# Optimization experiments

Hardware: AMD Instinct MI355X
Metric: run time of the kernel (lower is better)

Reference implementation:

```python
import jax, jax.numpy as jnp
import numpy as np

RADIUS = 2
TOP_K = 5000
SCORES_TH = 0.2
TEMPERATURE = 0.1


def setup_inputs() -> dict:
    key = jax.random.key(0)
    score_map = jax.random.uniform(key, (16, 1, 1024, 1024), dtype=jnp.float32)
    return {"score_map": score_map}


def _simple_nms(s, kernel_size):
    # max_pool2d(kernel, stride=1, pad=kernel//2) then keep only local maxima
    pad = kernel_size // 2
    mp = jax.lax.reduce_window(
        s, -jnp.inf, jax.lax.max,
        window_dimensions=(1, 1, kernel_size, kernel_size),
        window_strides=(1, 1, 1, 1),
        padding=((0, 0), (0, 0), (pad, pad), (pad, pad)))
    return jnp.where(s == mp, s, jnp.zeros_like(s))


def reference(score_map):
    B, _, H, W = score_map.shape
    ksize = 2 * RADIUS + 1

    # --- NMS (applied twice, as in the torch code) ---
    nms = score_map
    for _ in range(2):
        nms = _simple_nms(nms, ksize)

    # --- top-k + threshold ---
    flat = nms.reshape(B, -1)                      # (B, H*W)
    k = min(TOP_K, flat.shape[1])
    topk_scores, topk_idx = jax.lax.top_k(flat, k)  # sorted desc -> valid set is a prefix
    valid = topk_scores > SCORES_TH                 # (B, K)
    y_pix = topk_idx // W                           # (B, K) int
    x_pix = topk_idx % W

    # --- batched windowed soft-argmax refinement (boundary-aware) ---
    half = RADIUS
    d = jnp.arange(-half, half + 1)                 # (ksize,)
    dy = d[:, None] * jnp.ones((1, ksize), d.dtype) # (ksize, ksize)
    dx = d[None, :] * jnp.ones((ksize, 1), d.dtype)
    yy = y_pix[:, :, None, None] + dy               # (B, K, ksize, ksize)
    xx = x_pix[:, :, None, None] + dx
    inb = (yy >= 0) & (yy < H) & (xx >= 0) & (xx < W)
    yy_c = jnp.clip(yy, 0, H - 1)
    xx_c = jnp.clip(xx, 0, W - 1)

    sm = score_map[:, 0]                            # (B, H, W)
    b_idx = jnp.arange(B)[:, None, None, None]
    patch = sm[b_idx, yy_c, xx_c]                   # (B, K, ksize, ksize)

    # softmax over valid window entries only (out-of-bounds masked to -1e9,
    # equivalent to the torch code slicing away boundary pixels)
    logits = jnp.where(inb, patch / TEMPERATURE, jnp.float32(-1e9))
    wts = jax.nn.softmax(logits.reshape(B, k, -1), axis=-1)  # (B, K, ksize*ksize)

    dxf = dx.reshape(-1).astype(score_map.dtype)
    dyf = dy.reshape(-1).astype(score_map.dtype)
    off_x = jnp.einsum('bkw,w->bk', wts, dxf)
    off_y = jnp.einsum('bkw,w->bk', wts, dyf)

    kpts = jnp.stack([x_pix.astype(score_map.dtype) + off_x,
                      y_pix.astype(score_map.dtype) + off_y], axis=-1)  # (B, K, 2)

    # invalid (below-threshold) keypoints are zero-padded, matching the torch padding
    keypoints = jnp.where(valid[..., None], kpts, jnp.zeros_like(kpts))
    scores = jnp.where(valid, topk_scores, jnp.zeros_like(topk_scores))
    return keypoints, scores
```

## Files before the change

kernel.cpp:

```cpp
#include <hip/hip_runtime.h>
#include <math.h>

#define B 16
#define H 1024
#define W 1024
#define TOPK 5000
#define SCORES_TH 0.2f

#define SELCAP 8192
#define NB2 9831
#define OFFB2 510361
#define GS2 9840
#define SCHUNK 10

#define XSTRIPS 5
#define YSTRIPS 64
#define SROWS 16
#define SCOLS 252
#define WCAP 256
#define SLOTS (XSTRIPS * YSTRIPS)
#define CAPB (SLOTS * WCAP)

__global__ __launch_bounds__(256) void nms_wave(
    const float* __restrict__ s,
    unsigned* __restrict__ wc,
    unsigned long long* __restrict__ cand)
{
    __shared__ unsigned long long wbuf[4][WCAP];
    __shared__ unsigned wcnt[4];

    const int tid  = threadIdx.x;
    const int w    = tid >> 6;
    const int lane = tid & 63;
    const int gw   = blockIdx.x * 4 + w;
    const int xs   = gw % XSTRIPS;
    const int t    = gw / XSTRIPS;
    const int ys   = t & (YSTRIPS - 1);
    const int b    = t >> 6;
    const int slot = xs * YSTRIPS + ys;

    if (lane == 0) wcnt[w] = 0;

    const float* sb = s + (size_t)b * (H * W);
    const int c0 = xs * SCOLS - 2 + 4 * lane;
    const int y0 = ys * SROWS;
    const bool wfast = (xs > 0) & (xs < XSTRIPS - 1);

    bool inb[4], emitok[4];
    #pragma unroll
    for (int j = 0; j < 4; ++j) {
        int col = c0 + j, idx4 = 4 * lane + j;
        inb[j]    = (col >= 0) & (col < W);
        emitok[j] = inb[j] & (idx4 >= 2) & (idx4 <= 253);
    }

    float ring[4][4], p1[4], p2[4];
    #pragma unroll
    for (int j = 0; j < 4; ++j) {
        ring[j][0] = ring[j][1] = ring[j][2] = ring[j][3] = -INFINITY;
        p1[j] = p2[j] = -INFINITY;
    }

    #pragma unroll 4
    for (int gy = y0 - 2; gy <= y0 + SROWS + 1; ++gy) {
        float a[4];
        const bool yin = (gy >= 0) & (gy < H);
        if (yin & wfast) {
            float4 v = *(const float4*)(sb + (size_t)gy * W + c0);
            a[0] = v.x; a[1] = v.y; a[2] = v.z; a[3] = v.w;
        } else if (yin) {
            #pragma unroll
            for (int j = 0; j < 4; ++j)
                a[j] = inb[j] ? sb[(size_t)gy * W + c0 + j] : -INFINITY;
        } else {
            #pragma unroll
            for (int j = 0; j < 4; ++j) a[j] = -INFINITY;
        }

        float pm01 = fmaxf(a[0], a[1]);
        float pm12 = fmaxf(a[1], a[2]);
        float pm23 = fmaxf(a[2], a[3]);
        float Lh  = __shfl_up(pm23, 1);
        float La3 = __shfl_up(a[3], 1);
        float Ra0 = __shfl_down(a[0], 1);
        float Rp  = __shfl_down(pm01, 1);
        float h[4];
        h[0] = fmaxf(fmaxf(Lh,  pm01), a[2]);
        h[1] = fmaxf(fmaxf(La3, pm01), pm23);
        h[2] = fmaxf(fmaxf(pm01, pm23), Ra0);
        h[3] = fmaxf(fmaxf(pm12, pm23), Rp);

        if (gy >= y0 + 2) {
            const int r = gy - 2;
            #pragma unroll
            for (int j = 0; j < 4; ++j) {
                float vm = fmaxf(fmaxf(fmaxf(ring[j][0], ring[j][1]),
                                       fmaxf(ring[j][2], ring[j][3])), h[j]);
                bool pk = emitok[j] & (p2[j] > SCORES_TH) & (p2[j] == vm);
                if (pk) {
                    unsigned idx = (unsigned)(r * W + c0 + j);
                    unsigned long long key =
                        ((unsigned long long)__float_as_uint(p2[j]) << 32) | (unsigned)(~idx);
                    unsigned pi = atomicAdd(&wcnt[w], 1u);
                    if (pi < WCAP) wbuf[w][pi] = key;
                }
            }
        }

        #pragma unroll
        for (int j = 0; j < 4; ++j) {
            ring[j][0] = ring[j][1]; ring[j][1] = ring[j][2];
            ring[j][2] = ring[j][3]; ring[j][3] = h[j];
            p2[j] = p1[j]; p1[j] = a[j];
        }
    }

    unsigned n = wcnt[w]; if (n > WCAP) n = WCAP;
    const size_t base = (size_t)b * CAPB + (size_t)slot * WCAP;
    for (unsigned k = (unsigned)lane; k < n; k += 64)
        cand[base + k] = wbuf[w][k];
    if (lane == 0) wc[b * SLOTS + slot] = n;
}

__global__ __launch_bounds__(1024) void scan_scatter(
    const unsigned* __restrict__ wc,
    const unsigned long long* __restrict__ cand,
    unsigned* __restrict__ G,
    unsigned* __restrict__ selC,
    unsigned long long* __restrict__ sel)
{
    const int b = blockIdx.x;
    __shared__ unsigned I[NB2 + 1];
    __shared__ unsigned lwc[SLOTS];
    __shared__ unsigned wsum[16];
    __shared__ int Tsh;
    const int tid  = threadIdx.x;
    const int wv   = tid >> 6;
    const int lane = tid & 63;

    for (int i = tid; i < NB2 + 1; i += 1024) I[i] = 0;
    if (tid < SLOTS) {
        unsigned n = wc[b * SLOTS + tid];
        lwc[tid] = n > WCAP ? WCAP : n;
    }
    if (tid == 0) Tsh = 0;
    __syncthreads();

    const unsigned long long* cb = cand + (size_t)b * CAPB;

    for (unsigned i = (unsigned)tid; i < CAPB; i += 1024) {
        if ((i & (WCAP - 1)) < lwc[i >> 8]) {
            unsigned bits = (unsigned)(cb[i] >> 32);
            int bk = (int)(bits >> 11) - OFFB2;
            bk = bk < 0 ? 0 : (bk > NB2 - 1 ? NB2 - 1 : bk);
            atomicAdd(&I[bk], 1u);
        }
    }
    __syncthreads();

    unsigned local = 0;
    #pragma unroll
    for (int u = 0; u < SCHUNK; ++u) {
        int r = tid * SCHUNK + u;
        if (r < NB2) local += I[NB2 - 1 - r];
    }
    unsigned incl = local;
    #pragma unroll
    for (int off = 1; off < 64; off <<= 1) {
        unsigned v = __shfl_up(incl, off);
        if (lane >= off) incl += v;
    }
    if (lane == 63) wsum[wv] = incl;
    __syncthreads();
    if (tid < 16) {
        unsigned o = wsum[tid];
        unsigned x = o;
        #pragma unroll
        for (int off = 1; off < 16; off <<= 1) {
            unsigned v = __shfl_up(x, off);
            if (tid >= off) x += v;
        }
        wsum[tid] = x - o;
    }
    __syncthreads();
    unsigned run = wsum[wv] + (incl - local);
    #pragma unroll
    for (int u = 0; u < SCHUNK; ++u) {
        int r = tid * SCHUNK + u;
        if (r < NB2) {
            int bk = NB2 - 1 - r;
            run += I[bk];
            I[bk] = run;
        }
    }
    __syncthreads();

    int localT = -1;
    #pragma unroll
    for (int u = 0; u < SCHUNK; ++u) {
        int r = tid * SCHUNK + u;
        if (r < NB2) {
            int bk = NB2 - 1 - r;
            if (I[bk] >= TOPK && bk > localT) localT = bk;
        }
    }
    if (localT >= 0) atomicMax(&Tsh, localT);
    __syncthreads();
    const int T = Tsh;
    if (tid == 0) selC[b] = I[T];

    unsigned* Gb = G + (size_t)b * GS2;
    for (int i = tid; i < NB2 + 1; i += 1024) Gb[i] = I[i];
    __syncthreads();

    for (unsigned i = (unsigned)tid; i < CAPB; i += 1024) {
        if ((i & (WCAP - 1)) < lwc[i >> 8]) {
            unsigned long long key = cb[i];
            unsigned bits = (unsigned)(key >> 32);
            int bk = (int)(bits >> 11) - OFFB2;
            bk = bk < 0 ? 0 : (bk > NB2 - 1 ? NB2 - 1 : bk);
            if (bk >= T) {
                unsigned p = atomicAdd(&I[bk + 1], 1u);
                if (p < SELCAP) sel[(size_t)b * SELCAP + p] = key;
            }
        }
    }
}

__global__ __launch_bounds__(256) void rank_refine(
    const float* __restrict__ s,
    const unsigned long long* __restrict__ sel,
    const unsigned* __restrict__ selC,
    const unsigned* __restrict__ G,
    float* __restrict__ out)
{
    const int b = blockIdx.y;
    unsigned C = selC[b]; if (C > SELCAP) C = SELCAP;
    const int tid = threadIdx.x;
    const unsigned g = blockIdx.x * 64u + (unsigned)(tid >> 2);
    const int l = tid & 3;

    if (g >= C) {
        if (g < TOPK && l == 0) {
            out[((size_t)b * TOPK + g) * 2 + 0] = 0.0f;
            out[((size_t)b * TOPK + g) * 2 + 1] = 0.0f;
            out[(size_t)B * TOPK * 2 + (size_t)b * TOPK + g] = 0.0f;
        }
        return;
    }

    const unsigned long long* sb = sel + (size_t)b * SELCAP;
    const unsigned long long my = sb[g];
    unsigned bits = (unsigned)(my >> 32);
    int bk = (int)(bits >> 11) - OFFB2;
    bk = bk < 0 ? 0 : (bk > NB2 - 1 ? NB2 - 1 : bk);

    const unsigned* Gb = G + (size_t)b * GS2;
    unsigned start = Gb[bk + 1], end = Gb[bk];
    if (end > SELCAP) end = SELCAP;
    unsigned rank = 0;
    for (unsigned j = start + (unsigned)l; j < end; j += 4)
        rank += (sb[j] > my) ? 1u : 0u;

    float v = __uint_as_float(bits);
    unsigned idx = ~((unsigned)my);
    int y = (int)(idx >> 10), x = (int)(idx & 1023);
    const float* smb = s + (size_t)b * (H * W);
    float wsum = 0.f, ox = 0.f, oy = 0.f;
    for (int c = l; c < 25; c += 4) {
        int dy = c / 5 - 2, dx = c - (c / 5) * 5 - 2;
        int yy = y + dy, xx = x + dx;
        bool inb = (yy >= 0 && yy < H && xx >= 0 && xx < W);
        int yc = min(max(yy, 0), H - 1), xc = min(max(xx, 0), W - 1);
        float p = smb[yc * W + xc];
        float lg = inb ? p * 10.0f : -1e9f;
        float e = expf(lg);
        wsum += e; ox += e * (float)dx; oy += e * (float)dy;
    }
    rank += __shfl_xor(rank, 1); rank += __shfl_xor(rank, 2);
    wsum += __shfl_xor(wsum, 1); wsum += __shfl_xor(wsum, 2);
    ox   += __shfl_xor(ox, 1);   ox   += __shfl_xor(ox, 2);
    oy   += __shfl_xor(oy, 1);   oy   += __shfl_xor(oy, 2);

    unsigned frank = start + rank;
    if (l == 0 && frank < TOPK) {
        float offx = ox / wsum, offy = oy / wsum;
        out[((size_t)b * TOPK + frank) * 2 + 0] = (float)x + offx;
        out[((size_t)b * TOPK + frank) * 2 + 1] = (float)y + offy;
        out[(size_t)B * TOPK * 2 + (size_t)b * TOPK + frank] = v;
    }
}

extern "C" void kernel_launch(void* const* d_in, const int* in_sizes, int n_in,
                              void* d_out, int out_size, void* d_ws, size_t ws_size,
                              hipStream_t stream)
{
    const float* s = (const float*)d_in[0];
    float* out = (float*)d_out;
    char* ws = (char*)d_ws;

    size_t off = 0;
    unsigned* wc            = (unsigned*)(ws + off);  off += (size_t)B * SLOTS * 4;
    unsigned* selC          = (unsigned*)(ws + off);  off += 64;
    unsigned* G             = (unsigned*)(ws + off);  off += (size_t)B * GS2 * 4;
    unsigned long long* sel = (unsigned long long*)(ws + off); off += (size_t)B * SELCAP * 8;
    unsigned long long* cand= (unsigned long long*)(ws + off);

    nms_wave<<<dim3(XSTRIPS * YSTRIPS * B / 4), dim3(256), 0, stream>>>(s, wc, cand);
    scan_scatter<<<dim3(B), dim3(1024), 0, stream>>>(wc, cand, G, selC, sel);
    rank_refine<<<dim3(SELCAP * 4 / 256, B), dim3(256), 0, stream>>>(s, sel, selC, G, out);
}
```

Baseline: 103.5 us.

## Split scan_scatter into grid-wide histogram, scan, and scatter kernels

The single per-batch scan_scatter kernel used only 16 workgroups, each walking all candidate slots twice. It is now split into three kernels. hist_build and scatter_sel each launch one workgroup per slot and batch and use global atomics; the histogram is zeroed inside nms_wave. scanT computes the suffix sums and threshold bucket, and rank_refine reads bucket bounds shifted by one because the scatter advances the global offsets in place. This raises parallelism across the GPU in exchange for two extra launches and contended global atomics.

```diff
diff --git a/kernel.cpp b/kernel.cpp
--- a/kernel.cpp
+++ b/kernel.cpp
@@ -24,12 +24,19 @@
 __global__ __launch_bounds__(256) void nms_wave(
     const float* __restrict__ s,
     unsigned* __restrict__ wc,
-    unsigned long long* __restrict__ cand)
+    unsigned long long* __restrict__ cand,
+    unsigned* __restrict__ hist)
 {
     __shared__ unsigned long long wbuf[4][WCAP];
     __shared__ unsigned wcnt[4];
 
     const int tid  = threadIdx.x;
+
+    {
+        unsigned zi = blockIdx.x * 256u + (unsigned)tid;
+        if (zi < (unsigned)(B * GS2)) hist[zi] = 0u;
+    }
+
     const int w    = tid >> 6;
     const int lane = tid & 63;
     const int gw   = blockIdx.x * 4 + w;
@@ -122,40 +129,41 @@
     if (lane == 0) wc[b * SLOTS + slot] = n;
 }
 
-__global__ __launch_bounds__(1024) void scan_scatter(
+__global__ __launch_bounds__(256) void hist_build(
     const unsigned* __restrict__ wc,
     const unsigned long long* __restrict__ cand,
+    unsigned* __restrict__ hist)
+{
+    const int slot = blockIdx.x, b = blockIdx.y;
+    unsigned n = wc[b * SLOTS + slot]; if (n > WCAP) n = WCAP;
+    const unsigned tid = threadIdx.x;
+    if (tid < n) {
+        unsigned long long key = cand[(size_t)b * CAPB + (size_t)slot * WCAP + tid];
+        unsigned bits = (unsigned)(key >> 32);
+        int bk = (int)(bits >> 11) - OFFB2;
+        bk = bk < 0 ? 0 : (bk > NB2 - 1 ? NB2 - 1 : bk);
+        atomicAdd(&hist[(size_t)b * GS2 + bk], 1u);
+    }
+}
+
+__global__ __launch_bounds__(1024) void scanT(
+    const unsigned* __restrict__ hist,
     unsigned* __restrict__ G,
     unsigned* __restrict__ selC,
-    unsigned long long* __restrict__ sel)
+    unsigned* __restrict__ Tarr)
 {
     const int b = blockIdx.x;
-    __shared__ unsigned I[NB2 + 1];
-    __shared__ unsigned lwc[SLOTS];
+    __shared__ unsigned I[NB2 + 2];
     __shared__ unsigned wsum[16];
     __shared__ int Tsh;
     const int tid  = threadIdx.x;
     const int wv   = tid >> 6;
     const int lane = tid & 63;
-
-    for (int i = tid; i < NB2 + 1; i += 1024) I[i] = 0;
-    if (tid < SLOTS) {
-        unsigned n = wc[b * SLOTS + tid];
-        lwc[tid] = n > WCAP ? WCAP : n;
-    }
+    const unsigned* hb = hist + (size_t)b * GS2;
+
+    #pragma unroll 10
+    for (int i = tid; i < NB2 + 2; i += 1024) I[i] = (i < NB2) ? hb[i] : 0u;
     if (tid == 0) Tsh = 0;
-    __syncthreads();
-
-    const unsigned long long* cb = cand + (size_t)b * CAPB;
-
-    for (unsigned i = (unsigned)tid; i < CAPB; i += 1024) {
-        if ((i & (WCAP - 1)) < lwc[i >> 8]) {
-            unsigned bits = (unsigned)(cb[i] >> 32);
-            int bk = (int)(bits >> 11) - OFFB2;
-            bk = bk < 0 ? 0 : (bk > NB2 - 1 ? NB2 - 1 : bk);
-            atomicAdd(&I[bk], 1u);
-        }
-    }
     __syncthreads();
 
     unsigned local = 0;
@@ -207,22 +215,31 @@
     if (localT >= 0) atomicMax(&Tsh, localT);
     __syncthreads();
     const int T = Tsh;
-    if (tid == 0) selC[b] = I[T];
+    if (tid == 0) { selC[b] = I[T]; Tarr[b] = (unsigned)T; }
 
     unsigned* Gb = G + (size_t)b * GS2;
-    for (int i = tid; i < NB2 + 1; i += 1024) Gb[i] = I[i];
-    __syncthreads();
-
-    for (unsigned i = (unsigned)tid; i < CAPB; i += 1024) {
-        if ((i & (WCAP - 1)) < lwc[i >> 8]) {
-            unsigned long long key = cb[i];
-            unsigned bits = (unsigned)(key >> 32);
-            int bk = (int)(bits >> 11) - OFFB2;
-            bk = bk < 0 ? 0 : (bk > NB2 - 1 ? NB2 - 1 : bk);
-            if (bk >= T) {
-                unsigned p = atomicAdd(&I[bk + 1], 1u);
-                if (p < SELCAP) sel[(size_t)b * SELCAP + p] = key;
-            }
+    #pragma unroll 10
+    for (int i = tid; i < NB2 + 2; i += 1024) Gb[i] = I[i];
+}
+
+__global__ __launch_bounds__(256) void scatter_sel(
+    const unsigned* __restrict__ wc,
+    const unsigned long long* __restrict__ cand,
+    const unsigned* __restrict__ Tarr,
+    unsigned* __restrict__ G,
+    unsigned long long* __restrict__ sel)
+{
+    const int slot = blockIdx.x, b = blockIdx.y;
+    unsigned n = wc[b * SLOTS + slot]; if (n > WCAP) n = WCAP;
+    const unsigned tid = threadIdx.x;
+    if (tid < n) {
+        unsigned long long key = cand[(size_t)b * CAPB + (size_t)slot * WCAP + tid];
+        unsigned bits = (unsigned)(key >> 32);
+        int bk = (int)(bits >> 11) - OFFB2;
+        bk = bk < 0 ? 0 : (bk > NB2 - 1 ? NB2 - 1 : bk);
+        if (bk >= (int)Tarr[b]) {
+            unsigned p = atomicAdd(&G[(size_t)b * GS2 + bk + 1], 1u);
+            if (p < SELCAP) sel[(size_t)b * SELCAP + p] = key;
         }
     }
 }
@@ -256,7 +273,7 @@
     bk = bk < 0 ? 0 : (bk > NB2 - 1 ? NB2 - 1 : bk);
 
     const unsigned* Gb = G + (size_t)b * GS2;
-    unsigned start = Gb[bk + 1], end = Gb[bk];
+    unsigned start = Gb[bk + 2], end = Gb[bk + 1];
     if (end > SELCAP) end = SELCAP;
     unsigned rank = 0;
     for (unsigned j = start + (unsigned)l; j < end; j += 4)
@@ -302,11 +319,15 @@
     size_t off = 0;
     unsigned* wc            = (unsigned*)(ws + off);  off += (size_t)B * SLOTS * 4;
     unsigned* selC          = (unsigned*)(ws + off);  off += 64;
+    unsigned* Tarr          = (unsigned*)(ws + off);  off += 64;
     unsigned* G             = (unsigned*)(ws + off);  off += (size_t)B * GS2 * 4;
+    unsigned* hist          = (unsigned*)(ws + off);  off += (size_t)B * GS2 * 4;
     unsigned long long* sel = (unsigned long long*)(ws + off); off += (size_t)B * SELCAP * 8;
     unsigned long long* cand= (unsigned long long*)(ws + off);
 
-    nms_wave<<<dim3(XSTRIPS * YSTRIPS * B / 4), dim3(256), 0, stream>>>(s, wc, cand);
-    scan_scatter<<<dim3(B), dim3(1024), 0, stream>>>(wc, cand, G, selC, sel);
+    nms_wave<<<dim3(XSTRIPS * YSTRIPS * B / 4), dim3(256), 0, stream>>>(s, wc, cand, hist);
+    hist_build<<<dim3(SLOTS, B), dim3(256), 0, stream>>>(wc, cand, hist);
+    scanT<<<dim3(B), dim3(1024), 0, stream>>>(hist, G, selC, Tarr);
+    scatter_sel<<<dim3(SLOTS, B), dim3(256), 0, stream>>>(wc, cand, Tarr, G, sel);
     rank_refine<<<dim3(SELCAP * 4 / 256, B), dim3(256), 0, stream>>>(s, sel, selC, G, out);
 }
```

Result: slower. 139.9 us (+35.2%).
